# Performance work log

Measured on AMD Instinct MI355X. Metric: run time of the kernel, lower is better.

## Reference

```python
import jax, jax.numpy as jnp
import numpy as np

D = 2048      # token_dim (forced equal to visual feat dim by concat shapes)
V = 10000     # vocab size
B = 32        # batch
X = 36        # regions
T = 20        # max_len / caption length
FEAT = 2048


def setup_inputs() -> dict:
    key = jax.random.key(0)
    ks = jax.random.split(key, 20)
    s = 0.02
    inp = {
        "features": jax.random.normal(ks[0], (B, X, FEAT), jnp.float32),
        "caption": jax.random.randint(ks[1], (B, T), 0, V),
        "emb": jax.random.normal(ks[2], (V, D), jnp.float32) * s,
        # attention LSTMCell: input 3*D, hidden D
        "Wih_a": jax.random.normal(ks[3], (4 * D, 3 * D), jnp.float32) * s,
        "Whh_a": jax.random.normal(ks[4], (4 * D, D), jnp.float32) * s,
        "bih_a": jnp.zeros((4 * D,), jnp.float32),
        "bhh_a": jnp.zeros((4 * D,), jnp.float32),
        # language LSTMCell: input 2*D, hidden D
        "Wih_l": jax.random.normal(ks[5], (4 * D, 2 * D), jnp.float32) * s,
        "Whh_l": jax.random.normal(ks[6], (4 * D, D), jnp.float32) * s,
        "bih_l": jnp.zeros((4 * D,), jnp.float32),
        "bhh_l": jnp.zeros((4 * D,), jnp.float32),
        # attention MLP
        "Wv": jax.random.normal(ks[7], (D, FEAT), jnp.float32) * s,
        "bv": jnp.zeros((D,), jnp.float32),
        "Wh": jax.random.normal(ks[8], (D, D), jnp.float32) * s,
        "bh": jnp.zeros((D,), jnp.float32),
        "Wa": jax.random.normal(ks[9], (1, D), jnp.float32) * s,
        "ba": jnp.zeros((1,), jnp.float32),
        # output projection
        "Wfc": jax.random.normal(ks[10], (V, D), jnp.float32) * s,
        "bfc": jnp.zeros((V,), jnp.float32),
    }
    return inp


def _lstm_cell(x, h, c, Wih, Whh, bih, bhh):
    # PyTorch LSTMCell: gates in (i, f, g, o) order
    z = x @ Wih.T + bih + h @ Whh.T + bhh
    i, f, g, o = jnp.split(z, 4, axis=-1)
    c_new = jax.nn.sigmoid(f) * c + jax.nn.sigmoid(i) * jnp.tanh(g)
    h_new = jax.nn.sigmoid(o) * jnp.tanh(c_new)
    return h_new, c_new


def reference(features, caption, emb, Wih_a, Whh_a, bih_a, bhh_a,
              Wih_l, Whh_l, bih_l, bhh_l, Wv, bv, Wh, bh, Wa, ba, Wfc, bfc):
    v_bar = jnp.mean(features, axis=1)            # [B, 2048]
    embs = emb[caption]                            # [B, T, D]
    a_v = features @ Wv.T + bv                     # [B, X, D], t-invariant

    h0 = jnp.zeros((features.shape[0], D), features.dtype)
    carry0 = (h0, h0, h0, h0)  # (h_attn, c_attn, h_lang, c_lang)

    def step(carry, e_t):
        h_a, c_a, h_l, c_l = carry
        x = jnp.concatenate([h_l, v_bar, e_t], axis=1)          # [B, 3D]
        h_a, c_a = _lstm_cell(x, h_a, c_a, Wih_a, Whh_a, bih_a, bhh_a)
        # additive attention (NB: softmax over trailing singleton dim,
        # reproduced faithfully from the source -> weights are all ones)
        a_h = (h_a @ Wh.T + bh)[:, None, :]                      # [B, 1, D]
        a = jnp.tanh(a_v + a_h) @ Wa.T + ba                      # [B, X, 1]
        a_w = jax.nn.softmax(a, axis=-1)                         # [B, X, 1]
        v_hat = jnp.sum(a_w * features, axis=1)                  # [B, 2048]
        x2 = jnp.concatenate([h_a, v_hat], axis=1)               # [B, 2D]
        h_l, c_l = _lstm_cell(x2, h_l, c_l, Wih_l, Whh_l, bih_l, bhh_l)
        logits_t = h_l @ Wfc.T + bfc                             # [B, V]
        return (h_a, c_a, h_l, c_l), logits_t

    _, logits = jax.lax.scan(step, carry0, jnp.swapaxes(embs, 0, 1))  # [T, B, V]
    logits = jnp.swapaxes(logits, 0, 1)                               # [B, T, V]
    return jax.nn.log_softmax(logits, axis=2)
```

## Files before the change

### kernel.cpp

```cpp
#include <hip/hip_runtime.h>

typedef unsigned short u16;
typedef __attribute__((ext_vector_type(8))) short bf16x8;
typedef __attribute__((ext_vector_type(4))) float f32x4;

#define DD 2048
#define VV 10000
#define BB 32
#define TT 20

__device__ __forceinline__ u16 f2bf(float f) {
    unsigned u = __float_as_uint(f);
    u += 0x7fffu + ((u >> 16) & 1u);
    return (u16)(u >> 16);
}
__device__ __forceinline__ float bf2f(u16 h) {
    return __uint_as_float(((unsigned)h) << 16);
}

__global__ __launch_bounds__(256) void cast_weights(
    const float* __restrict__ Wih_a, const float* __restrict__ Whh_a,
    const float* __restrict__ Wih_l, const float* __restrict__ Whh_l,
    const float* __restrict__ Wfc,
    u16* __restrict__ Wcat_a, u16* __restrict__ Wcat_l, u16* __restrict__ Wfc_b)
{
    const long long S1 = 8192LL * 4096;
    const long long S3P = 10016LL * 2048;
    long long g = (long long)blockIdx.x * 256 + threadIdx.x;
    long long e = g * 4;
    const float* src;
    u16* dst;
    if (e < S1) {
        int n = (int)(e >> 12), k = (int)(e & 4095);
        src = (k < 2048) ? (Wih_a + (size_t)n * 6144 + k)
                         : (Whh_a + (size_t)n * 2048 + (k - 2048));
        dst = Wcat_a + e;
    } else if (e < 2 * S1) {
        long long e2 = e - S1;
        int n = (int)(e2 >> 12), k = (int)(e2 & 4095);
        src = (k < 2048) ? (Wih_l + (size_t)n * 4096 + k)
                         : (Whh_l + (size_t)n * 2048 + (k - 2048));
        dst = Wcat_l + e2;
    } else {
        long long e3 = e - 2 * S1;
        if (e3 >= S3P) return;
        dst = Wfc_b + e3;
        int row = (int)(e3 >> 11);
        if (row >= VV) {
            ushort4 z; z.x = 0; z.y = 0; z.z = 0; z.w = 0;
            *(ushort4*)dst = z;
            return;
        }
        src = Wfc + e3;
    }
    float4 v = *(const float4*)src;
    ushort4 o;
    o.x = f2bf(v.x); o.y = f2bf(v.y); o.z = f2bf(v.z); o.w = f2bf(v.w);
    *(ushort4*)dst = o;
}

__global__ __launch_bounds__(256) void prep(
    const float* __restrict__ features,
    u16* __restrict__ vbar, u16* __restrict__ vhat,
    float* __restrict__ c_a, float* __restrict__ c_l,
    u16* __restrict__ Ha0, u16* __restrict__ Hl0)
{
    int i = blockIdx.x * 256 + threadIdx.x;
    int b = i >> 11, d = i & 2047;
    const float* f = features + (size_t)b * 36 * 2048 + d;
    float s = 0.f;
#pragma unroll
    for (int x = 0; x < 36; ++x) s += f[(size_t)x * 2048];
    vhat[i] = f2bf(s);
    vbar[i] = f2bf(s * (1.f / 36.f));
    c_a[i] = 0.f; c_l[i] = 0.f;
    Ha0[i] = 0;  Hl0[i] = 0;
}

__global__ __launch_bounds__(256) void embed_k(
    const float* __restrict__ emb, const int* __restrict__ caption,
    u16* __restrict__ embs)
{
    int i = blockIdx.x * 256 + threadIdx.x;
    int m = i >> 11, d = i & 2047;
    int t = m >> 5, b = m & 31;
    int tok = caption[b * TT + t];
    embs[i] = f2bf(emb[(size_t)tok * 2048 + d]);
}

template <int MT>
__global__ __launch_bounds__(256) void pre_gemm(
    const u16* __restrict__ A, const float* __restrict__ W,
    int ldw, int kofs,
    const float* __restrict__ bias0, const float* __restrict__ bias1,
    float* __restrict__ out)
{
    const int lane = threadIdx.x & 63;
    const int wv = threadIdx.x >> 6;
    const int lr = lane & 15, lq = lane >> 4;
    const int n0 = blockIdx.x * 64 + wv * 16;
    const int m0 = blockIdx.y * (MT * 16);

    f32x4 acc[MT];
#pragma unroll
    for (int i = 0; i < MT; ++i) acc[i] = (f32x4){0.f, 0.f, 0.f, 0.f};

    const float* wrow = W + (size_t)(n0 + lr) * ldw + kofs + lq * 8;
    const u16* arow = A + (size_t)(m0 + lr) * 2048 + lq * 8;

    for (int k = 0; k < 2048; k += 32) {
        float4 wlo = *(const float4*)(wrow + k);
        float4 whi = *(const float4*)(wrow + k + 4);
        bf16x8 bf;
        bf[0] = (short)f2bf(wlo.x); bf[1] = (short)f2bf(wlo.y);
        bf[2] = (short)f2bf(wlo.z); bf[3] = (short)f2bf(wlo.w);
        bf[4] = (short)f2bf(whi.x); bf[5] = (short)f2bf(whi.y);
        bf[6] = (short)f2bf(whi.z); bf[7] = (short)f2bf(whi.w);
#pragma unroll
        for (int mt = 0; mt < MT; ++mt) {
            bf16x8 af = *(const bf16x8*)(arow + (size_t)mt * 16 * 2048 + k);
            acc[mt] = __builtin_amdgcn_mfma_f32_16x16x32_bf16(af, bf, acc[mt], 0, 0, 0);
        }
    }
    const int n = n0 + lr;
    float badd = 0.f;
    if (bias0) badd += bias0[n];
    if (bias1) badd += bias1[n];
#pragma unroll
    for (int mt = 0; mt < MT; ++mt) {
#pragma unroll
        for (int r = 0; r < 4; ++r) {
            int m = m0 + mt * 16 + lq * 4 + r;
            out[(size_t)m * 8192 + n] = acc[mt][r] + badd;
        }
    }
}

__global__ __launch_bounds__(512) void step_kernel(
    const u16* __restrict__ A0, const u16* __restrict__ A1,
    const u16* __restrict__ W, const float* __restrict__ zconst,
    float* __restrict__ c, u16* __restrict__ hout)
{
    __shared__ float zred[8][32][17];
    const int tid = threadIdx.x;
    const int lane = tid & 63;
    const int w = tid >> 6;
    const int lr = lane & 15, lq = lane >> 4;
    const int d0 = blockIdx.x * 4;

    const int g = lr >> 2, dd = lr & 3;
    const int nrow = g * 2048 + d0 + dd;

    const u16* Aptr = (w < 4) ? A0 : A1;
    const int kA = (w & 3) * 512 + lq * 8;

    const u16* ar0 = Aptr + (size_t)lr * 2048 + kA;
    const u16* ar1 = ar0 + 16 * 2048;
    bf16x8 af0[16], af1[16];
#pragma unroll
    for (int kk = 0; kk < 16; ++kk) {
        af0[kk] = *(const bf16x8*)(ar0 + kk * 32);
        af1[kk] = *(const bf16x8*)(ar1 + kk * 32);
    }

    const u16* wrow = W + (size_t)nrow * 4096 + w * 512 + lq * 8;
    f32x4 acc0 = (f32x4){0.f, 0.f, 0.f, 0.f};
    f32x4 acc1 = (f32x4){0.f, 0.f, 0.f, 0.f};
    bf16x8 wf[8];
#pragma unroll
    for (int kk = 0; kk < 8; ++kk)
        wf[kk] = *(const bf16x8*)(wrow + kk * 32);
#pragma unroll
    for (int kk = 0; kk < 16; ++kk) {
        acc0 = __builtin_amdgcn_mfma_f32_16x16x32_bf16(af0[kk], wf[kk & 7], acc0, 0, 0, 0);
        acc1 = __builtin_amdgcn_mfma_f32_16x16x32_bf16(af1[kk], wf[kk & 7], acc1, 0, 0, 0);
        if (kk < 8)
            wf[kk] = *(const bf16x8*)(wrow + (kk + 8) * 32);
    }

#pragma unroll
    for (int r = 0; r < 4; ++r) {
        zred[w][lq * 4 + r][lr]      = acc0[r];
        zred[w][16 + lq * 4 + r][lr] = acc1[r];
    }
    __syncthreads();

    if (tid < 128) {
        const int b = tid >> 2;
        const int j = tid & 3;
        const int d = d0 + j;
        float z[4];
#pragma unroll
        for (int gg = 0; gg < 4; ++gg) {
            float s = zconst[(size_t)b * 8192 + gg * 2048 + d];
#pragma unroll
            for (int wv = 0; wv < 8; ++wv) s += zred[wv][b][gg * 4 + j];
            z[gg] = s;
        }
        float ig = 1.f / (1.f + __expf(-z[0]));
        float fg = 1.f / (1.f + __expf(-z[1]));
        float gv = tanhf(z[2]);
        float og = 1.f / (1.f + __expf(-z[3]));
        float cn = fg * c[(size_t)b * 2048 + d] + ig * gv;
        c[(size_t)b * 2048 + d] = cn;
        hout[(size_t)b * 2048 + d] = f2bf(og * tanhf(cn));
    }
}

template <int MODE>
__global__ __launch_bounds__(256) void big_gemm(
    const u16* __restrict__ A, const void* __restrict__ Wp,
    const float* __restrict__ extra, float* __restrict__ out)
{
    const int NWN = MODE ? 313 : 256;
    const int nwg = MODE ? 783 : 640;
    int bid = blockIdx.x;
    {
        int q = nwg >> 3, r = nwg & 7, x = bid & 7, o = bid >> 3;
        bid = (x < r ? x * (q + 1) : r * (q + 1) + (x - r) * q) + o;
    }
    const int gw = bid * 4 + (int)(threadIdx.x >> 6);
    const int wm = gw % 10;
    const int wn = gw / 10;
    if (wn >= NWN) return;
    const int lane = threadIdx.x & 63;
    const int lr = lane & 15, lq = lane >> 4;
    const int m0 = wm * 64, n0 = wn * 32;

    f32x4 acc[4][2];
#pragma unroll
    for (int mt = 0; mt < 4; ++mt)
#pragma unroll
        for (int nt = 0; nt < 2; ++nt) acc[mt][nt] = (f32x4){0.f, 0.f, 0.f, 0.f};

    const u16* arow = A + (size_t)(m0 + lr) * 2048 + lq * 8;

    if (MODE == 1) {
        const u16* Wb = (const u16*)Wp;
        const u16* wrow0 = Wb + (size_t)(n0 + lr) * 2048 + lq * 8;
        const u16* wrow1 = wrow0 + 16 * 2048;
#pragma unroll 2
        for (int k = 0; k < 2048; k += 32) {
            bf16x8 w0 = *(const bf16x8*)(wrow0 + k);
            bf16x8 w1 = *(const bf16x8*)(wrow1 + k);
#pragma unroll
            for (int mt = 0; mt < 4; ++mt) {
                bf16x8 a = *(const bf16x8*)(arow + (size_t)mt * 16 * 2048 + k);
                acc[mt][0] = __builtin_amdgcn_mfma_f32_16x16x32_bf16(a, w0, acc[mt][0], 0, 0, 0);
                acc[mt][1] = __builtin_amdgcn_mfma_f32_16x16x32_bf16(a, w1, acc[mt][1], 0, 0, 0);
            }
        }
    } else {
        const float* Wf = (const float*)Wp;
        const float* wrow0 = Wf + (size_t)(n0 + lr) * 6144 + 4096 + lq * 8;
        const float* wrow1 = wrow0 + (size_t)16 * 6144;
#pragma unroll 2
        for (int k = 0; k < 2048; k += 32) {
            float4 p0 = *(const float4*)(wrow0 + k);
            float4 p1 = *(const float4*)(wrow0 + k + 4);
            float4 q0 = *(const float4*)(wrow1 + k);
            float4 q1 = *(const float4*)(wrow1 + k + 4);
            bf16x8 w0, w1;
            w0[0] = (short)f2bf(p0.x); w0[1] = (short)f2bf(p0.y);
            w0[2] = (short)f2bf(p0.z); w0[3] = (short)f2bf(p0.w);
            w0[4] = (short)f2bf(p1.x); w0[5] = (short)f2bf(p1.y);
            w0[6] = (short)f2bf(p1.z); w0[7] = (short)f2bf(p1.w);
            w1[0] = (short)f2bf(q0.x); w1[1] = (short)f2bf(q0.y);
            w1[2] = (short)f2bf(q0.z); w1[3] = (short)f2bf(q0.w);
            w1[4] = (short)f2bf(q1.x); w1[5] = (short)f2bf(q1.y);
            w1[6] = (short)f2bf(q1.z); w1[7] = (short)f2bf(q1.w);
#pragma unroll
            for (int mt = 0; mt < 4; ++mt) {
                bf16x8 a = *(const bf16x8*)(arow + (size_t)mt * 16 * 2048 + k);
                acc[mt][0] = __builtin_amdgcn_mfma_f32_16x16x32_bf16(a, w0, acc[mt][0], 0, 0, 0);
                acc[mt][1] = __builtin_amdgcn_mfma_f32_16x16x32_bf16(a, w1, acc[mt][1], 0, 0, 0);
            }
        }
    }

#pragma unroll
    for (int mt = 0; mt < 4; ++mt) {
#pragma unroll
        for (int nt = 0; nt < 2; ++nt) {
            const int n = n0 + nt * 16 + lr;
#pragma unroll
            for (int r = 0; r < 4; ++r) {
                const int m = m0 + mt * 16 + lq * 4 + r;
                if (MODE == 0) {
                    out[(size_t)m * 8192 + n] =
                        acc[mt][nt][r] + extra[(size_t)(m & 31) * 8192 + n];
                } else {
                    if (n < VV) {
                        const int t = m >> 5, b = m & 31;
                        out[(size_t)b * (TT * VV) + (size_t)t * VV + n] =
                            acc[mt][nt][r] + extra[n];
                    }
                }
            }
        }
    }
}

__global__ __launch_bounds__(256) void logsoftmax(float* __restrict__ out)
{
    float* p = out + (size_t)blockIdx.x * VV;
    const int tid = threadIdx.x, lane = tid & 63, wv = tid >> 6;
    __shared__ float red[4], red2[4];
    float mx = -1e30f;
    for (int i = tid; i < VV; i += 256) mx = fmaxf(mx, p[i]);
    for (int o = 32; o > 0; o >>= 1) mx = fmaxf(mx, __shfl_down(mx, o, 64));
    if (lane == 0) red[wv] = mx;
    __syncthreads();
    mx = fmaxf(fmaxf(red[0], red[1]), fmaxf(red[2], red[3]));
    float sum = 0.f;
    for (int i = tid; i < VV; i += 256) sum += __expf(p[i] - mx);
    for (int o = 32; o > 0; o >>= 1) sum += __shfl_down(sum, o, 64);
    if (lane == 0) red2[wv] = sum;
    __syncthreads();
    sum = red2[0] + red2[1] + red2[2] + red2[3];
    const float lse = mx + __logf(sum);
    for (int i = tid; i < VV; i += 256) p[i] = p[i] - lse;
}

extern "C" void kernel_launch(void* const* d_in, const int* in_sizes, int n_in,
                              void* d_out, int out_size, void* d_ws, size_t ws_size,
                              hipStream_t stream)
{
    const float* features = (const float*)d_in[0];
    const int*   caption  = (const int*)d_in[1];
    const float* emb      = (const float*)d_in[2];
    const float* Wih_a    = (const float*)d_in[3];
    const float* Whh_a    = (const float*)d_in[4];
    const float* bih_a    = (const float*)d_in[5];
    const float* bhh_a    = (const float*)d_in[6];
    const float* Wih_l    = (const float*)d_in[7];
    const float* Whh_l    = (const float*)d_in[8];
    const float* bih_l    = (const float*)d_in[9];
    const float* bhh_l    = (const float*)d_in[10];
    const float* Wfc      = (const float*)d_in[17];
    const float* bfc      = (const float*)d_in[18];
    float* out = (float*)d_out;

    char* ws = (char*)d_ws;
    size_t off = 0;
    auto alloc = [&](size_t bytes) { void* p = ws + off; off += (bytes + 255) & ~(size_t)255; return p; };
    u16* Wcat_a  = (u16*)alloc(8192ull * 4096 * 2);
    u16* Wcat_l  = (u16*)alloc(8192ull * 4096 * 2);
    u16* Wfc_b   = (u16*)alloc(10016ull * 2048 * 2);
    float* z_const = (float*)alloc(20ull * 32 * 8192 * 4);
    float* const_a = (float*)alloc(32ull * 8192 * 4);
    float* const_l = (float*)alloc(32ull * 8192 * 4);
    u16* embs    = (u16*)alloc(640ull * 2048 * 2);
    u16* vbar    = (u16*)alloc(32ull * 2048 * 2);
    u16* vhat    = (u16*)alloc(32ull * 2048 * 2);
    u16* Ha      = (u16*)alloc(2ull * 32 * 2048 * 2);
    u16* Hl      = (u16*)alloc(21ull * 32 * 2048 * 2);
    float* c_a   = (float*)alloc(32ull * 2048 * 4);
    float* c_l   = (float*)alloc(32ull * 2048 * 4);
    (void)ws_size; (void)in_sizes; (void)n_in; (void)out_size;

    cast_weights<<<dim3(85568), dim3(256), 0, stream>>>(
        Wih_a, Whh_a, Wih_l, Whh_l, Wfc, Wcat_a, Wcat_l, Wfc_b);
    prep<<<dim3(256), dim3(256), 0, stream>>>(features, vbar, vhat, c_a, c_l, Ha, Hl);
    embed_k<<<dim3(5120), dim3(256), 0, stream>>>(emb, caption, embs);
    pre_gemm<2><<<dim3(128, 1), dim3(256), 0, stream>>>(
        vbar, Wih_a, 6144, 2048, bih_a, bhh_a, const_a);
    pre_gemm<2><<<dim3(128, 1), dim3(256), 0, stream>>>(
        vhat, Wih_l, 4096, 2048, bih_l, bhh_l, const_l);
    big_gemm<0><<<dim3(640), dim3(256), 0, stream>>>(
        embs, (const void*)Wih_a, const_a, z_const);

    for (int t = 0; t < 20; ++t) {
        u16* hl_prev = Hl + (size_t)t * 65536;
        u16* ha_prev = Ha + (size_t)(t & 1) * 65536;
        u16* ha_new  = Ha + (size_t)((t + 1) & 1) * 65536;
        u16* hl_new  = Hl + (size_t)(t + 1) * 65536;
        step_kernel<<<dim3(512), dim3(512), 0, stream>>>(
            hl_prev, ha_prev, Wcat_a, z_const + (size_t)t * 262144, c_a, ha_new);
        step_kernel<<<dim3(512), dim3(512), 0, stream>>>(
            ha_new, hl_prev, Wcat_l, const_l, c_l, hl_new);
    }

    big_gemm<1><<<dim3(783), dim3(256), 0, stream>>>(
        Hl + 65536, (const void*)Wfc_b, bfc, out);
    logsoftmax<<<dim3(640), dim3(256), 0, stream>>>(out);
}
```

Baseline: 2.028 ms.

## Pre-pack all weights into MFMA fragment order and unify GEMMs

Weights are now cast to bf16 in a layout matching the MFMA lane fragment order, so each wave reads contiguous 16-byte chunks instead of strided rows. The vbar and embedding GEMMs are merged into one K=4096 GEMM over an augmented activation matrix, which removes on-the-fly fp32-to-bf16 weight conversion in the pre-GEMMs. The step kernel computes 8 hidden units per block with 256 blocks instead of 4 units with 512 blocks. The cost is a larger packing pass and more workspace, since the Wih_a and Wih_l input slices are packed separately.

```diff
diff --git a/kernel.cpp b/kernel.cpp
--- a/kernel.cpp
+++ b/kernel.cpp
@@ -14,49 +14,82 @@
     u += 0x7fffu + ((u >> 16) & 1u);
     return (u16)(u >> 16);
 }
-__device__ __forceinline__ float bf2f(u16 h) {
-    return __uint_as_float(((unsigned)h) << 16);
-}
-
-__global__ __launch_bounds__(256) void cast_weights(
+
+__global__ __launch_bounds__(256) void pack_weights(
     const float* __restrict__ Wih_a, const float* __restrict__ Whh_a,
     const float* __restrict__ Wih_l, const float* __restrict__ Whh_l,
     const float* __restrict__ Wfc,
-    u16* __restrict__ Wcat_a, u16* __restrict__ Wcat_l, u16* __restrict__ Wfc_b)
-{
-    const long long S1 = 8192LL * 4096;
-    const long long S3P = 10016LL * 2048;
-    long long g = (long long)blockIdx.x * 256 + threadIdx.x;
-    long long e = g * 4;
+    u16* __restrict__ Wcat_a, u16* __restrict__ Wcat_l,
+    u16* __restrict__ Wfc_p, u16* __restrict__ Wza_p, u16* __restrict__ Wcl_p)
+{
+    const size_t E0 = 33554432ull;
+    const size_t E1 = 67108864ull;
+    const size_t E2 = 87621632ull;
+    const size_t E3 = 121176064ull;
+    const size_t E4 = 137953280ull;
+    size_t ph = ((size_t)blockIdx.x * 256 + threadIdx.x) * 8;
+    if (ph >= E4) return;
     const float* src;
     u16* dst;
-    if (e < S1) {
-        int n = (int)(e >> 12), k = (int)(e & 4095);
-        src = (k < 2048) ? (Wih_a + (size_t)n * 6144 + k)
-                         : (Whh_a + (size_t)n * 2048 + (k - 2048));
-        dst = Wcat_a + e;
-    } else if (e < 2 * S1) {
-        long long e2 = e - S1;
-        int n = (int)(e2 >> 12), k = (int)(e2 & 4095);
-        src = (k < 2048) ? (Wih_l + (size_t)n * 4096 + k)
-                         : (Whh_l + (size_t)n * 2048 + (k - 2048));
-        dst = Wcat_l + e2;
+    if (ph < E1) {
+        size_t p = ph;
+        const float* Wih = Wih_a; const float* Whh = Whh_a;
+        size_t ldw = 6144;
+        u16* base = Wcat_a;
+        if (p >= E0) { p -= E0; Wih = Wih_l; Whh = Whh_l; ldw = 4096; base = Wcat_l; }
+        int lane = (int)((p >> 3) & 63), lr = lane & 15, lq = lane >> 4;
+        int nt = (int)((p >> 9) & 1);
+        int kk = (int)((p >> 10) & 15);
+        int w  = (int)((p >> 14) & 7);
+        int blk = (int)(p >> 17);
+        int n = (lr >> 2) * 2048 + blk * 8 + nt * 4 + (lr & 3);
+        int k = w * 512 + kk * 32 + lq * 8;
+        src = (k < 2048) ? (Wih + (size_t)n * ldw + k)
+                         : (Whh + (size_t)n * 2048 + (k - 2048));
+        dst = base + p;
+    } else if (ph < E2) {
+        size_t p = ph - E1;
+        int lane = (int)((p >> 3) & 63), lr = lane & 15, lq = lane >> 4;
+        int nt = (int)((p >> 9) & 1);
+        int ks = (int)((p >> 10) & 63);
+        int wn = (int)(p >> 16);
+        int n = wn * 32 + nt * 16 + lr;
+        int k = ks * 32 + lq * 8;
+        dst = Wfc_p + p;
+        if (n >= VV) {
+            ushort4 z; z.x = 0; z.y = 0; z.z = 0; z.w = 0;
+            *(ushort4*)dst = z; *(ushort4*)(dst + 4) = z;
+            return;
+        }
+        src = Wfc + (size_t)n * 2048 + k;
+    } else if (ph < E3) {
+        size_t p = ph - E2;
+        int lane = (int)((p >> 3) & 63), lr = lane & 15, lq = lane >> 4;
+        int nt = (int)((p >> 9) & 1);
+        int ks = (int)((p >> 10) & 127);
+        int wn = (int)(p >> 17);
+        int n = wn * 32 + nt * 16 + lr;
+        int k = ks * 32 + lq * 8;
+        src = Wih_a + (size_t)n * 6144 + 2048 + k;
+        dst = Wza_p + p;
     } else {
-        long long e3 = e - 2 * S1;
-        if (e3 >= S3P) return;
-        dst = Wfc_b + e3;
-        int row = (int)(e3 >> 11);
-        if (row >= VV) {
-            ushort4 z; z.x = 0; z.y = 0; z.z = 0; z.w = 0;
-            *(ushort4*)dst = z;
-            return;
-        }
-        src = Wfc + e3;
-    }
-    float4 v = *(const float4*)src;
-    ushort4 o;
-    o.x = f2bf(v.x); o.y = f2bf(v.y); o.z = f2bf(v.z); o.w = f2bf(v.w);
-    *(ushort4*)dst = o;
+        size_t p = ph - E3;
+        int lane = (int)((p >> 3) & 63), lr = lane & 15, lq = lane >> 4;
+        int nt = (int)((p >> 9) & 1);
+        int ks = (int)((p >> 10) & 63);
+        int wn = (int)(p >> 16);
+        int n = wn * 32 + nt * 16 + lr;
+        int k = ks * 32 + lq * 8;
+        src = Wih_l + (size_t)n * 4096 + 2048 + k;
+        dst = Wcl_p + p;
+    }
+    float4 lo = *(const float4*)src;
+    float4 hi = *(const float4*)(src + 4);
+    ushort4 o0, o1;
+    o0.x = f2bf(lo.x); o0.y = f2bf(lo.y); o0.z = f2bf(lo.z); o0.w = f2bf(lo.w);
+    o1.x = f2bf(hi.x); o1.y = f2bf(hi.y); o1.z = f2bf(hi.z); o1.w = f2bf(hi.w);
+    *(ushort4*)dst = o0;
+    *(ushort4*)(dst + 4) = o1;
 }
 
 __global__ __launch_bounds__(256) void prep(
@@ -77,79 +110,108 @@
     Ha0[i] = 0;  Hl0[i] = 0;
 }
 
-__global__ __launch_bounds__(256) void embed_k(
+__global__ __launch_bounds__(256) void embed_aug(
     const float* __restrict__ emb, const int* __restrict__ caption,
-    u16* __restrict__ embs)
-{
-    int i = blockIdx.x * 256 + threadIdx.x;
-    int m = i >> 11, d = i & 2047;
+    const u16* __restrict__ vbar, u16* __restrict__ A_aug)
+{
+    int idx = blockIdx.x * 256 + threadIdx.x;
+    int m = idx >> 9;
+    int col8 = (idx & 511) * 8;
     int t = m >> 5, b = m & 31;
-    int tok = caption[b * TT + t];
-    embs[i] = f2bf(emb[(size_t)tok * 2048 + d]);
-}
-
-template <int MT>
-__global__ __launch_bounds__(256) void pre_gemm(
-    const u16* __restrict__ A, const float* __restrict__ W,
-    int ldw, int kofs,
-    const float* __restrict__ bias0, const float* __restrict__ bias1,
+    u16* dst = A_aug + (size_t)m * 4096 + col8;
+    if (col8 < 2048) {
+        ushort4 v0 = *(const ushort4*)(vbar + (size_t)b * 2048 + col8);
+        ushort4 v1 = *(const ushort4*)(vbar + (size_t)b * 2048 + col8 + 4);
+        *(ushort4*)dst = v0; *(ushort4*)(dst + 4) = v1;
+    } else {
+        int tok = caption[b * TT + t];
+        const float* s = emb + (size_t)tok * 2048 + (col8 - 2048);
+        float4 lo = *(const float4*)s, hi = *(const float4*)(s + 4);
+        ushort4 o0, o1;
+        o0.x = f2bf(lo.x); o0.y = f2bf(lo.y); o0.z = f2bf(lo.z); o0.w = f2bf(lo.w);
+        o1.x = f2bf(hi.x); o1.y = f2bf(hi.y); o1.z = f2bf(hi.z); o1.w = f2bf(hi.w);
+        *(ushort4*)dst = o0; *(ushort4*)(dst + 4) = o1;
+    }
+}
+
+template <int KS, int NWN, int NM, int MT, int MODE>
+__global__ __launch_bounds__(256) void gemm_p(
+    const u16* __restrict__ A, const u16* __restrict__ Wp,
+    const float* __restrict__ b0, const float* __restrict__ b1,
     float* __restrict__ out)
 {
+    const int K = KS * 32;
+    const int nwaves = NM * NWN;
+    const int nwg = (nwaves + 3) >> 2;
+    int bid = blockIdx.x;
+    {
+        int q = nwg >> 3, r = nwg & 7, x = bid & 7, o = bid >> 3;
+        bid = (x < r ? x * (q + 1) : r * (q + 1) + (x - r) * q) + o;
+    }
+    const int gw = bid * 4 + (int)(threadIdx.x >> 6);
+    if (gw >= nwaves) return;
+    const int wm = gw % NM, wn = gw / NM;
     const int lane = threadIdx.x & 63;
-    const int wv = threadIdx.x >> 6;
     const int lr = lane & 15, lq = lane >> 4;
-    const int n0 = blockIdx.x * 64 + wv * 16;
-    const int m0 = blockIdx.y * (MT * 16);
-
-    f32x4 acc[MT];
-#pragma unroll
-    for (int i = 0; i < MT; ++i) acc[i] = (f32x4){0.f, 0.f, 0.f, 0.f};
-
-    const float* wrow = W + (size_t)(n0 + lr) * ldw + kofs + lq * 8;
-    const u16* arow = A + (size_t)(m0 + lr) * 2048 + lq * 8;
-
-    for (int k = 0; k < 2048; k += 32) {
-        float4 wlo = *(const float4*)(wrow + k);
-        float4 whi = *(const float4*)(wrow + k + 4);
-        bf16x8 bf;
-        bf[0] = (short)f2bf(wlo.x); bf[1] = (short)f2bf(wlo.y);
-        bf[2] = (short)f2bf(wlo.z); bf[3] = (short)f2bf(wlo.w);
-        bf[4] = (short)f2bf(whi.x); bf[5] = (short)f2bf(whi.y);
-        bf[6] = (short)f2bf(whi.z); bf[7] = (short)f2bf(whi.w);
+    const int m0 = wm * (MT * 16);
+
+    f32x4 acc[MT][2];
+#pragma unroll
+    for (int mt = 0; mt < MT; ++mt) {
+        acc[mt][0] = (f32x4){0.f, 0.f, 0.f, 0.f};
+        acc[mt][1] = (f32x4){0.f, 0.f, 0.f, 0.f};
+    }
+    const u16* arow = A + (size_t)(m0 + lr) * K + lq * 8;
+    const u16* wptr = Wp + (size_t)wn * (KS * 1024) + lane * 8;
+
+#pragma unroll 4
+    for (int ks = 0; ks < KS; ++ks) {
+        bf16x8 w0 = *(const bf16x8*)(wptr + (size_t)ks * 1024);
+        bf16x8 w1 = *(const bf16x8*)(wptr + (size_t)ks * 1024 + 512);
 #pragma unroll
         for (int mt = 0; mt < MT; ++mt) {
-            bf16x8 af = *(const bf16x8*)(arow + (size_t)mt * 16 * 2048 + k);
-            acc[mt] = __builtin_amdgcn_mfma_f32_16x16x32_bf16(af, bf, acc[mt], 0, 0, 0);
-        }
-    }
-    const int n = n0 + lr;
-    float badd = 0.f;
-    if (bias0) badd += bias0[n];
-    if (bias1) badd += bias1[n];
-#pragma unroll
-    for (int mt = 0; mt < MT; ++mt) {
-#pragma unroll
-        for (int r = 0; r < 4; ++r) {
-            int m = m0 + mt * 16 + lq * 4 + r;
-            out[(size_t)m * 8192 + n] = acc[mt][r] + badd;
-        }
-    }
-}
-
-__global__ __launch_bounds__(512) void step_kernel(
+            bf16x8 a = *(const bf16x8*)(arow + (size_t)mt * 16 * K + ks * 32);
+            acc[mt][0] = __builtin_amdgcn_mfma_f32_16x16x32_bf16(a, w0, acc[mt][0], 0, 0, 0);
+            acc[mt][1] = __builtin_amdgcn_mfma_f32_16x16x32_bf16(a, w1, acc[mt][1], 0, 0, 0);
+        }
+    }
+
+#pragma unroll
+    for (int nt = 0; nt < 2; ++nt) {
+        const int n = wn * 32 + nt * 16 + lr;
+        float badd = 0.f;
+        if (b0) badd += b0[n < (MODE ? VV : 8192) ? n : 0];
+        if (b1) badd += b1[n < 8192 ? n : 0];
+#pragma unroll
+        for (int mt = 0; mt < MT; ++mt) {
+#pragma unroll
+            for (int r = 0; r < 4; ++r) {
+                const int m = m0 + mt * 16 + lq * 4 + r;
+                float v = acc[mt][nt][r] + badd;
+                if (MODE == 0) {
+                    out[(size_t)m * 8192 + n] = v;
+                } else {
+                    if (n < VV) {
+                        const int t = m >> 5, b = m & 31;
+                        out[(size_t)b * (TT * VV) + (size_t)t * VV + n] = v;
+                    }
+                }
+            }
+        }
+    }
+}
+
+__global__ __launch_bounds__(512, 2) void step_kernel(
     const u16* __restrict__ A0, const u16* __restrict__ A1,
-    const u16* __restrict__ W, const float* __restrict__ zconst,
+    const u16* __restrict__ Wp, const float* __restrict__ zconst,
     float* __restrict__ c, u16* __restrict__ hout)
 {
-    __shared__ float zred[8][32][17];
+    __shared__ float zred[8][32][33];
     const int tid = threadIdx.x;
     const int lane = tid & 63;
     const int w = tid >> 6;
     const int lr = lane & 15, lq = lane >> 4;
-    const int d0 = blockIdx.x * 4;
-
-    const int g = lr >> 2, dd = lr & 3;
-    const int nrow = g * 2048 + d0 + dd;
+    const int blk = blockIdx.x;
 
     const u16* Aptr = (w < 4) ? A0 : A1;
     const int kA = (w & 3) * 512 + lq * 8;
@@ -163,38 +225,52 @@
         af1[kk] = *(const bf16x8*)(ar1 + kk * 32);
     }
 
-    const u16* wrow = W + (size_t)nrow * 4096 + w * 512 + lq * 8;
-    f32x4 acc0 = (f32x4){0.f, 0.f, 0.f, 0.f};
-    f32x4 acc1 = (f32x4){0.f, 0.f, 0.f, 0.f};
-    bf16x8 wf[8];
-#pragma unroll
-    for (int kk = 0; kk < 8; ++kk)
-        wf[kk] = *(const bf16x8*)(wrow + kk * 32);
+    const u16* wbase = Wp + ((size_t)blk * 8 + w) * 16384 + lane * 8;
+    f32x4 acc[2][2];
+    acc[0][0] = (f32x4){0.f, 0.f, 0.f, 0.f};
+    acc[0][1] = (f32x4){0.f, 0.f, 0.f, 0.f};
+    acc[1][0] = (f32x4){0.f, 0.f, 0.f, 0.f};
+    acc[1][1] = (f32x4){0.f, 0.f, 0.f, 0.f};
+    bf16x8 wf[8][2];
+#pragma unroll
+    for (int kk = 0; kk < 8; ++kk) {
+        wf[kk][0] = *(const bf16x8*)(wbase + kk * 1024);
+        wf[kk][1] = *(const bf16x8*)(wbase + kk * 1024 + 512);
+    }
 #pragma unroll
     for (int kk = 0; kk < 16; ++kk) {
-        acc0 = __builtin_amdgcn_mfma_f32_16x16x32_bf16(af0[kk], wf[kk & 7], acc0, 0, 0, 0);
-        acc1 = __builtin_amdgcn_mfma_f32_16x16x32_bf16(af1[kk], wf[kk & 7], acc1, 0, 0, 0);
-        if (kk < 8)
-            wf[kk] = *(const bf16x8*)(wrow + (kk + 8) * 32);
-    }
-
-#pragma unroll
-    for (int r = 0; r < 4; ++r) {
-        zred[w][lq * 4 + r][lr]      = acc0[r];
-        zred[w][16 + lq * 4 + r][lr] = acc1[r];
-    }
+        bf16x8 w0 = wf[kk & 7][0];
+        bf16x8 w1 = wf[kk & 7][1];
+        if (kk < 8) {
+            wf[kk][0] = *(const bf16x8*)(wbase + (kk + 8) * 1024);
+            wf[kk][1] = *(const bf16x8*)(wbase + (kk + 8) * 1024 + 512);
+        }
+        acc[0][0] = __builtin_amdgcn_mfma_f32_16x16x32_bf16(af0[kk], w0, acc[0][0], 0, 0, 0);
+        acc[1][0] = __builtin_amdgcn_mfma_f32_16x16x32_bf16(af1[kk], w0, acc[1][0], 0, 0, 0);
+        acc[0][1] = __builtin_amdgcn_mfma_f32_16x16x32_bf16(af0[kk], w1, acc[0][1], 0, 0, 0);
+        acc[1][1] = __builtin_amdgcn_mfma_f32_16x16x32_bf16(af1[kk], w1, acc[1][1], 0, 0, 0);
+    }
+
+#pragma unroll
+    for (int nt = 0; nt < 2; ++nt)
+#pragma unroll
+        for (int r = 0; r < 4; ++r) {
+            zred[w][lq * 4 + r][nt * 16 + lr]      = acc[0][nt][r];
+            zred[w][16 + lq * 4 + r][nt * 16 + lr] = acc[1][nt][r];
+        }
     __syncthreads();
 
-    if (tid < 128) {
-        const int b = tid >> 2;
-        const int j = tid & 3;
-        const int d = d0 + j;
+    if (tid < 256) {
+        const int b = tid >> 3;
+        const int j = tid & 7;
+        const int d = blk * 8 + j;
         float z[4];
 #pragma unroll
         for (int gg = 0; gg < 4; ++gg) {
+            const int col = (j >> 2) * 16 + gg * 4 + (j & 3);
             float s = zconst[(size_t)b * 8192 + gg * 2048 + d];
 #pragma unroll
-            for (int wv = 0; wv < 8; ++wv) s += zred[wv][b][gg * 4 + j];
+            for (int wv = 0; wv < 8; ++wv) s += zred[wv][b][col];
             z[gg] = s;
         }
         float ig = 1.f / (1.f + __expf(-z[0]));
@@ -204,100 +280,6 @@
         float cn = fg * c[(size_t)b * 2048 + d] + ig * gv;
         c[(size_t)b * 2048 + d] = cn;
         hout[(size_t)b * 2048 + d] = f2bf(og * tanhf(cn));
-    }
-}
-
-template <int MODE>
-__global__ __launch_bounds__(256) void big_gemm(
-    const u16* __restrict__ A, const void* __restrict__ Wp,
-    const float* __restrict__ extra, float* __restrict__ out)
-{
-    const int NWN = MODE ? 313 : 256;
-    const int nwg = MODE ? 783 : 640;
-    int bid = blockIdx.x;
-    {
-        int q = nwg >> 3, r = nwg & 7, x = bid & 7, o = bid >> 3;
-        bid = (x < r ? x * (q + 1) : r * (q + 1) + (x - r) * q) + o;
-    }
-    const int gw = bid * 4 + (int)(threadIdx.x >> 6);
-    const int wm = gw % 10;
-    const int wn = gw / 10;
-    if (wn >= NWN) return;
-    const int lane = threadIdx.x & 63;
-    const int lr = lane & 15, lq = lane >> 4;
-    const int m0 = wm * 64, n0 = wn * 32;
-
-    f32x4 acc[4][2];
-#pragma unroll
-    for (int mt = 0; mt < 4; ++mt)
-#pragma unroll
-        for (int nt = 0; nt < 2; ++nt) acc[mt][nt] = (f32x4){0.f, 0.f, 0.f, 0.f};
-
-    const u16* arow = A + (size_t)(m0 + lr) * 2048 + lq * 8;
-
-    if (MODE == 1) {
-        const u16* Wb = (const u16*)Wp;
-        const u16* wrow0 = Wb + (size_t)(n0 + lr) * 2048 + lq * 8;
-        const u16* wrow1 = wrow0 + 16 * 2048;
-#pragma unroll 2
-        for (int k = 0; k < 2048; k += 32) {
-            bf16x8 w0 = *(const bf16x8*)(wrow0 + k);
-            bf16x8 w1 = *(const bf16x8*)(wrow1 + k);
-#pragma unroll
-            for (int mt = 0; mt < 4; ++mt) {
-                bf16x8 a = *(const bf16x8*)(arow + (size_t)mt * 16 * 2048 + k);
-                acc[mt][0] = __builtin_amdgcn_mfma_f32_16x16x32_bf16(a, w0, acc[mt][0], 0, 0, 0);
-                acc[mt][1] = __builtin_amdgcn_mfma_f32_16x16x32_bf16(a, w1, acc[mt][1], 0, 0, 0);
-            }
-        }
-    } else {
-        const float* Wf = (const float*)Wp;
-        const float* wrow0 = Wf + (size_t)(n0 + lr) * 6144 + 4096 + lq * 8;
-        const float* wrow1 = wrow0 + (size_t)16 * 6144;
-#pragma unroll 2
-        for (int k = 0; k < 2048; k += 32) {
-            float4 p0 = *(const float4*)(wrow0 + k);
-            float4 p1 = *(const float4*)(wrow0 + k + 4);
-            float4 q0 = *(const float4*)(wrow1 + k);
-            float4 q1 = *(const float4*)(wrow1 + k + 4);
-            bf16x8 w0, w1;
-            w0[0] = (short)f2bf(p0.x); w0[1] = (short)f2bf(p0.y);
-            w0[2] = (short)f2bf(p0.z); w0[3] = (short)f2bf(p0.w);
-            w0[4] = (short)f2bf(p1.x); w0[5] = (short)f2bf(p1.y);
-            w0[6] = (short)f2bf(p1.z); w0[7] = (short)f2bf(p1.w);
-            w1[0] = (short)f2bf(q0.x); w1[1] = (short)f2bf(q0.y);
-            w1[2] = (short)f2bf(q0.z); w1[3] = (short)f2bf(q0.w);
-            w1[4] = (short)f2bf(q1.x); w1[5] = (short)f2bf(q1.y);
-            w1[6] = (short)f2bf(q1.z); w1[7] = (short)f2bf(q1.w);
-#pragma unroll
-            for (int mt = 0; mt < 4; ++mt) {
-                bf16x8 a = *(const bf16x8*)(arow + (size_t)mt * 16 * 2048 + k);
-                acc[mt][0] = __builtin_amdgcn_mfma_f32_16x16x32_bf16(a, w0, acc[mt][0], 0, 0, 0);
-                acc[mt][1] = __builtin_amdgcn_mfma_f32_16x16x32_bf16(a, w1, acc[mt][1], 0, 0, 0);
-            }
-        }
-    }
-
-#pragma unroll
-    for (int mt = 0; mt < 4; ++mt) {
-#pragma unroll
-        for (int nt = 0; nt < 2; ++nt) {
-            const int n = n0 + nt * 16 + lr;
-#pragma unroll
-            for (int r = 0; r < 4; ++r) {
-                const int m = m0 + mt * 16 + lq * 4 + r;
-                if (MODE == 0) {
-                    out[(size_t)m * 8192 + n] =
-                        acc[mt][nt][r] + extra[(size_t)(m & 31) * 8192 + n];
-                } else {
-                    if (n < VV) {
-                        const int t = m >> 5, b = m & 31;
-                        out[(size_t)b * (TT * VV) + (size_t)t * VV + n] =
-                            acc[mt][nt][r] + extra[n];
-                    }
-                }
-            }
-        }
     }
 }
 
@@ -344,13 +326,14 @@
     char* ws = (char*)d_ws;
     size_t off = 0;
     auto alloc = [&](size_t bytes) { void* p = ws + off; off += (bytes + 255) & ~(size_t)255; return p; };
-    u16* Wcat_a  = (u16*)alloc(8192ull * 4096 * 2);
-    u16* Wcat_l  = (u16*)alloc(8192ull * 4096 * 2);
-    u16* Wfc_b   = (u16*)alloc(10016ull * 2048 * 2);
+    u16* Wcat_a  = (u16*)alloc(33554432ull * 2);
+    u16* Wcat_l  = (u16*)alloc(33554432ull * 2);
+    u16* Wfc_p   = (u16*)alloc(20512768ull * 2);
+    u16* Wza_p   = (u16*)alloc(33554432ull * 2);
+    u16* Wcl_p   = (u16*)alloc(16777216ull * 2);
     float* z_const = (float*)alloc(20ull * 32 * 8192 * 4);
-    float* const_a = (float*)alloc(32ull * 8192 * 4);
     float* const_l = (float*)alloc(32ull * 8192 * 4);
-    u16* embs    = (u16*)alloc(640ull * 2048 * 2);
+    u16* A_aug   = (u16*)alloc(640ull * 4096 * 2);
     u16* vbar    = (u16*)alloc(32ull * 2048 * 2);
     u16* vhat    = (u16*)alloc(32ull * 2048 * 2);
     u16* Ha      = (u16*)alloc(2ull * 32 * 2048 * 2);
@@ -359,29 +342,27 @@
     float* c_l   = (float*)alloc(32ull * 2048 * 4);
     (void)ws_size; (void)in_sizes; (void)n_in; (void)out_size;
 
-    cast_weights<<<dim3(85568), dim3(256), 0, stream>>>(
-        Wih_a, Whh_a, Wih_l, Whh_l, Wfc, Wcat_a, Wcat_l, Wfc_b);
+    pack_weights<<<dim3(67360), dim3(256), 0, stream>>>(
+        Wih_a, Whh_a, Wih_l, Whh_l, Wfc, Wcat_a, Wcat_l, Wfc_p, Wza_p, Wcl_p);
     prep<<<dim3(256), dim3(256), 0, stream>>>(features, vbar, vhat, c_a, c_l, Ha, Hl);
-    embed_k<<<dim3(5120), dim3(256), 0, stream>>>(emb, caption, embs);
-    pre_gemm<2><<<dim3(128, 1), dim3(256), 0, stream>>>(
-        vbar, Wih_a, 6144, 2048, bih_a, bhh_a, const_a);
-    pre_gemm<2><<<dim3(128, 1), dim3(256), 0, stream>>>(
-        vhat, Wih_l, 4096, 2048, bih_l, bhh_l, const_l);
-    big_gemm<0><<<dim3(640), dim3(256), 0, stream>>>(
-        embs, (const void*)Wih_a, const_a, z_const);
+    embed_aug<<<dim3(1280), dim3(256), 0, stream>>>(emb, caption, vbar, A_aug);
+    gemm_p<64, 256, 1, 2, 0><<<dim3(64), dim3(256), 0, stream>>>(
+        vhat, Wcl_p, bih_l, bhh_l, const_l);
+    gemm_p<128, 256, 10, 4, 0><<<dim3(640), dim3(256), 0, stream>>>(
+        A_aug, Wza_p, bih_a, bhh_a, z_const);
 
     for (int t = 0; t < 20; ++t) {
         u16* hl_prev = Hl + (size_t)t * 65536;
         u16* ha_prev = Ha + (size_t)(t & 1) * 65536;
         u16* ha_new  = Ha + (size_t)((t + 1) & 1) * 65536;
         u16* hl_new  = Hl + (size_t)(t + 1) * 65536;
-        step_kernel<<<dim3(512), dim3(512), 0, stream>>>(
+        step_kernel<<<dim3(256), dim3(512), 0, stream>>>(
             hl_prev, ha_prev, Wcat_a, z_const + (size_t)t * 262144, c_a, ha_new);
-        step_kernel<<<dim3(512), dim3(512), 0, stream>>>(
+        step_kernel<<<dim3(256), dim3(512), 0, stream>>>(
             ha_new, hl_prev, Wcat_l, const_l, c_l, hl_new);
     }
 
-    big_gemm<1><<<dim3(783), dim3(256), 0, stream>>>(
-        Hl + 65536, (const void*)Wfc_b, bfc, out);
+    gemm_p<64, 313, 10, 4, 1><<<dim3(783), dim3(256), 0, stream>>>(
+        Hl + 65536, Wfc_p, bfc, nullptr, out);
     logsoftmax<<<dim3(640), dim3(256), 0, stream>>>(out);
 }
```

Result: faster. 1.736 ms (-14.4%).
